# Kernel tuning notes

Measured on AMD Instinct MI355X. Metric: run time of the kernel, lower is better.

Reference implementation:

```python
import jax, jax.numpy as jnp
import numpy as np

N, E = 50000, 800000
NI, NH, NO, NA = 64, 64, 64, 8
C_WEIGHT = 1.0


def psi(p):
    return jnp.sign(p) * jnp.log(jnp.abs(p) + 1.0)


def batchnorm(x, gamma, beta, eps=1e-5):
    # torch BatchNorm1d (training mode): biased variance over the batch dim
    mu = jnp.mean(x, axis=0)
    var = jnp.var(x, axis=0)
    return (x - mu) / jnp.sqrt(var + eps) * gamma + beta


def setup_inputs() -> dict:
    key = jax.random.key(0)
    ks = jax.random.split(key, 16)
    f32 = jnp.float32

    def w(k, shape, s):
        return jax.random.normal(k, shape, dtype=f32) * s

    inp = {}
    inp["h"] = jax.random.normal(ks[0], (N, NI), dtype=f32)
    inp["x"] = jax.random.normal(ks[1], (N, 4), dtype=f32)
    inp["edge_i"] = jax.random.randint(ks[2], (E,), 0, N)
    inp["edge_j"] = jax.random.randint(ks[3], (E,), 0, N)
    inp["node_attr"] = jax.random.normal(ks[4], (N, NA), dtype=f32)
    # phi_e: Linear(2*NI+2 -> NH, no bias), BN, ReLU, Linear(NH -> NH), ReLU
    inp["W_e1"] = w(ks[5], (2 * NI + 2, NH), 0.1)
    inp["g_e"] = jnp.ones((NH,), f32)
    inp["b_e"] = jnp.zeros((NH,), f32)
    inp["W_e2"] = w(ks[6], (NH, NH), 0.1)
    inp["b_e2"] = jnp.zeros((NH,), f32)
    # phi_m: Linear(NH -> 1), Sigmoid
    inp["W_m"] = w(ks[7], (NH, 1), 0.1)
    inp["b_m"] = jnp.zeros((1,), f32)
    # phi_x: Linear(NH -> NH), ReLU, Linear(NH -> 1, no bias, xavier gain=0.001)
    inp["W_x1"] = w(ks[8], (NH, NH), 0.1)
    inp["b_x1"] = jnp.zeros((NH,), f32)
    inp["W_x2"] = w(ks[9], (NH, 1), 0.0003)
    # phi_h: Linear(NH+NI+NA -> NH), BN, ReLU, Linear(NH -> NO)
    inp["W_h1"] = w(ks[10], (NH + NI + NA, NH), 0.1)
    inp["b_h1"] = jnp.zeros((NH,), f32)
    inp["g_h"] = jnp.ones((NH,), f32)
    inp["b_h"] = jnp.zeros((NH,), f32)
    inp["W_h2"] = w(ks[11], (NH, NO), 0.1)
    inp["b_h2"] = jnp.zeros((NO,), f32)
    return inp


def reference(h, x, edge_i, edge_j, node_attr,
              W_e1, g_e, b_e, W_e2, b_e2,
              W_m, b_m, W_x1, b_x1, W_x2,
              W_h1, b_h1, g_h, b_h, W_h2, b_h2):
    n_nodes = h.shape[0]
    xi = x[edge_i]            # [E, 4]
    xj = x[edge_j]            # [E, 4]
    x_diff = xi - xj
    # Minkowski norm / dot: 2*p0*q0 - sum(p*q)
    psq = x_diff * x_diff
    norms = psi(2.0 * psq[:, 0] - psq.sum(axis=-1))[:, None]   # [E,1]
    pq = xi * xj
    dots = psi(2.0 * pq[:, 0] - pq.sum(axis=-1))[:, None]      # [E,1]
    # m_model
    feat = jnp.concatenate([h[edge_i], h[edge_j], norms, dots], axis=1)  # [E, 2*NI+2]
    out = jax.nn.relu(batchnorm(feat @ W_e1, g_e, b_e))
    out = jax.nn.relu(out @ W_e2 + b_e2)
    w_gate = jax.nn.sigmoid(out @ W_m + b_m)
    m = out * w_gate                                            # [E, NH]
    # x_model
    phx = jax.nn.relu(m @ W_x1 + b_x1) @ W_x2                   # [E, 1]
    trans = jnp.clip(x_diff * phx, -100.0, 100.0)
    agg_x = jax.ops.segment_sum(trans, edge_i, num_segments=n_nodes)
    cnt = jax.ops.segment_sum(jnp.ones((trans.shape[0],), trans.dtype),
                              edge_i, num_segments=n_nodes)
    x_new = x + (agg_x / jnp.maximum(cnt, 1.0)[:, None]) * C_WEIGHT
    # h_model
    agg_h = jax.ops.segment_sum(m, edge_i, num_segments=n_nodes)
    hin = jnp.concatenate([h, agg_h, node_attr], axis=1)        # [N, NH+NI+NA]
    hh = jax.nn.relu(batchnorm(hin @ W_h1 + b_h1, g_h, b_h))
    h_new = h + (hh @ W_h2 + b_h2)
    return (h_new, x_new, m)
```

## Files before the change

### kernel.cpp

```cpp
#include <hip/hip_runtime.h>
#include <stdint.h>

typedef __attribute__((ext_vector_type(8))) short bf16x8;
typedef __attribute__((ext_vector_type(4))) float f32x4;

static constexpr int NN = 50000;
static constexpr int NE = 800000;

static constexpr int O_ESUM = 0;
static constexpr int O_ESQ  = 64;
static constexpr int O_HSUM = 128;
static constexpr int O_HSQ  = 192;
static constexpr int O_CNT  = 512;
static constexpr int O_ROW  = O_CNT + 50048;
static constexpr int O_CUR  = O_ROW + 50048;
static constexpr int O_BSUM = O_CUR + 50048;
static constexpr int O_CSR  = O_BSUM + 64;
static constexpr int O_PHX  = O_CSR + NE;
static constexpr int O_AGGH = O_PHX + NE;
static constexpr int O_YH   = O_AGGH + NN*64;
static constexpr int O_PQ   = O_YH + NN*64;
static constexpr int O_YB   = O_PQ + NN*64;
static constexpr int O_ND   = O_YB + NE*32;

static constexpr int OUT_X = NN*64;
static constexpr int OUT_M = NN*64 + NN*4;

__device__ __forceinline__ short f2bf(float f){
  uint32_t u = __builtin_bit_cast(uint32_t, f);
  u = (u + 0x7fffu + ((u >> 16) & 1u)) >> 16;
  return (short)u;
}
__device__ __forceinline__ float bflo(uint32_t w){ return __builtin_bit_cast(float, w << 16); }
__device__ __forceinline__ float bfhi(uint32_t w){ return __builtin_bit_cast(float, w & 0xffff0000u); }
__device__ __forceinline__ float psi_f(float p){
  return copysignf(__logf(fabsf(p) + 1.0f), p);
}
__device__ __forceinline__ bf16x8 ldrow8(const float* p){
  float4 p0 = *(const float4*)p;
  float4 p1 = *(const float4*)(p + 4);
  bf16x8 a;
  a[0]=f2bf(p0.x); a[1]=f2bf(p0.y); a[2]=f2bf(p0.z); a[3]=f2bf(p0.w);
  a[4]=f2bf(p1.x); a[5]=f2bf(p1.y); a[6]=f2bf(p1.z); a[7]=f2bf(p1.w);
  return a;
}

__global__ __launch_bounds__(256) void k_pq(
    const float* __restrict__ h, const float* __restrict__ We1,
    ushort* __restrict__ P, ushort* __restrict__ Q,
    int* __restrict__ cnt, float* __restrict__ wsf)
{
  __shared__ __align__(16) ushort sT[4][1024];
  const int lane = threadIdx.x & 63, wid = threadIdx.x >> 6;
  const int g = lane >> 4, q = lane & 15;
  const int ro = lane >> 2, cb = lane & 3;

  if (blockIdx.x == 0 && threadIdx.x < 256) wsf[threadIdx.x] = 0.f;

  bf16x8 wt[2][4], wm[2][4];
#pragma unroll
  for (int kb=0;kb<2;kb++)
#pragma unroll
    for (int nb=0;nb<4;nb++)
#pragma unroll
      for (int j=0;j<8;j++){
        wt[kb][nb][j] = f2bf(We1[(32*kb + 8*g + j)*64 + 16*nb + q]);
        wm[kb][nb][j] = f2bf(We1[(64 + 32*kb + 8*g + j)*64 + 16*nb + q]);
      }

  ushort* tb = sT[wid];
  const int gw = blockIdx.x*4 + wid, nw = gridDim.x*4;
  for (int t = gw; t < NN/16; t += nw){
    const int rb = t*16;
    if (lane < 16) cnt[rb + lane] = 0;
    const float* hp = h + (size_t)(rb+q)*64;
    bf16x8 a[2];
    a[0] = ldrow8(hp + 8*g); a[1] = ldrow8(hp + 32 + 8*g);

    f32x4 accP[4], accQ[4];
#pragma unroll
    for (int nb=0;nb<4;nb++){ accP[nb] = (f32x4){0.f,0.f,0.f,0.f}; accQ[nb] = (f32x4){0.f,0.f,0.f,0.f}; }
#pragma unroll
    for (int kb=0;kb<2;kb++)
#pragma unroll
      for (int nb=0;nb<4;nb++){
        accP[nb] = __builtin_amdgcn_mfma_f32_16x16x32_bf16(a[kb], wt[kb][nb], accP[nb], 0,0,0);
        accQ[nb] = __builtin_amdgcn_mfma_f32_16x16x32_bf16(a[kb], wm[kb][nb], accQ[nb], 0,0,0);
      }

    asm volatile("s_waitcnt lgkmcnt(0)" ::: "memory");
#pragma unroll
    for (int nb=0;nb<4;nb++)
#pragma unroll
      for (int r=0;r<4;r++){
        const int mr = 4*g + r;
        tb[mr*64 + ((16*nb + q) ^ ((mr&7)<<3))] = (ushort)f2bf(accP[nb][r]);
      }
    asm volatile("s_waitcnt lgkmcnt(0)" ::: "memory");
    {
      const int s = ro & 7;
      uint4 c0 = *(const uint4*)(tb + ro*64 + ((cb*16    ) ^ (s<<3)));
      uint4 c1 = *(const uint4*)(tb + ro*64 + ((cb*16 + 8) ^ (s<<3)));
      *(uint4*)(P + (size_t)(rb+ro)*64 + cb*16    ) = c0;
      *(uint4*)(P + (size_t)(rb+ro)*64 + cb*16 + 8) = c1;
    }
    asm volatile("s_waitcnt lgkmcnt(0)" ::: "memory");
#pragma unroll
    for (int nb=0;nb<4;nb++)
#pragma unroll
      for (int r=0;r<4;r++){
        const int mr = 4*g + r;
        tb[mr*64 + ((16*nb + q) ^ ((mr&7)<<3))] = (ushort)f2bf(accQ[nb][r]);
      }
    asm volatile("s_waitcnt lgkmcnt(0)" ::: "memory");
    {
      const int s = ro & 7;
      uint4 c0 = *(const uint4*)(tb + ro*64 + ((cb*16    ) ^ (s<<3)));
      uint4 c1 = *(const uint4*)(tb + ro*64 + ((cb*16 + 8) ^ (s<<3)));
      *(uint4*)(Q + (size_t)(rb+ro)*64 + cb*16    ) = c0;
      *(uint4*)(Q + (size_t)(rb+ro)*64 + cb*16 + 8) = c1;
    }
  }
}

__global__ __launch_bounds__(256) void k_nd(
    const float* __restrict__ x,
    const int* __restrict__ ei, const int* __restrict__ ej,
    float2* __restrict__ nd, int* __restrict__ cnt)
{
  const int stride = gridDim.x*256;
  for (int e = blockIdx.x*256 + threadIdx.x; e < NE; e += stride){
    const int i = ei[e], j = ej[e];
    const float4 xi = *(const float4*)(x + 4*i);
    const float4 xj = *(const float4*)(x + 4*j);
    const float dx=xi.x-xj.x, dy=xi.y-xj.y, dz=xi.z-xj.z, dw=xi.w-xj.w;
    float2 v;
    v.x = psi_f(dx*dx - dy*dy - dz*dz - dw*dw);
    v.y = psi_f(xi.x*xj.x - xi.y*xj.y - xi.z*xj.z - xi.w*xj.w);
    nd[e] = v;
    atomicAdd(cnt + i, 1);
  }
}

__global__ __launch_bounds__(256) void k_e1(
    const ushort* __restrict__ P, const ushort* __restrict__ Q,
    const int* __restrict__ ei, const int* __restrict__ ej,
    const float2* __restrict__ nd,
    const float* __restrict__ We1,
    ushort* __restrict__ yb, float* __restrict__ wsf)
{
  __shared__ float sred[8][64];
  const int lane = threadIdx.x & 63, wid = threadIdx.x >> 6;
  const float wn = We1[128*64 + lane];
  const float wd = We1[129*64 + lane];
  float ssum = 0.f, ssq = 0.f;

  const int gw = blockIdx.x*4 + wid, nw = gridDim.x*4;
  for (int t = gw; t < NE/8; t += nw){
    const int eb = __builtin_amdgcn_readfirstlane(t*8);
    int iv[8], jv[8];
    float nr[8], dt[8];
#pragma unroll
    for (int k=0;k<8;k++){
      iv[k] = ei[eb+k];
      jv[k] = ej[eb+k];
      const float2 v = nd[eb+k];
      nr[k] = v.x; dt[k] = v.y;
    }
    uint32_t pv[8], qv[8];
#pragma unroll
    for (int k=0;k<8;k++) pv[k] = P[(size_t)iv[k]*64 + lane];
#pragma unroll
    for (int k=0;k<8;k++) qv[k] = Q[(size_t)jv[k]*64 + lane];
#pragma unroll
    for (int k=0;k<8;k++){
      const float y = bflo(pv[k]) + bflo(qv[k]) + nr[k]*wn + dt[k]*wd;
      ssum += y; ssq += y*y;
      yb[(size_t)(eb+k)*64 + lane] = (ushort)f2bf(y);
    }
  }
  sred[wid][lane] = ssum;
  sred[4+wid][lane] = ssq;
  __syncthreads();
  if (wid == 0){
    const float s = sred[0][lane]+sred[1][lane]+sred[2][lane]+sred[3][lane];
    const float z = sred[4][lane]+sred[5][lane]+sred[6][lane]+sred[7][lane];
    atomicAdd(wsf + O_ESUM + lane, s);
    atomicAdd(wsf + O_ESQ  + lane, z);
  }
}

__global__ __launch_bounds__(1024) void k_scan_a(const int* __restrict__ cnt, int* __restrict__ row1,
                                                 int* __restrict__ bsum, int n){
  int v = blockIdx.x*1024 + threadIdx.x;
  int x = (v < n) ? cnt[v] : 0;
  const int lane = threadIdx.x & 63, wid = threadIdx.x >> 6;
#pragma unroll
  for (int d=1; d<64; d<<=1){ int y = __shfl_up(x, d, 64); if (lane >= d) x += y; }
  __shared__ int ws[16];
  if (lane == 63) ws[wid] = x;
  __syncthreads();
  if (wid == 0){
    int s = (lane < 16) ? ws[lane] : 0;
#pragma unroll
    for (int d=1; d<16; d<<=1){ int y = __shfl_up(s, d, 64); if (lane >= d) s += y; }
    if (lane < 16) ws[lane] = s;
  }
  __syncthreads();
  if (wid > 0) x += ws[wid-1];
  if (v < n) row1[v] = x;
  if (threadIdx.x == 1023) bsum[blockIdx.x] = x;
}

__global__ void k_scan_b(int* __restrict__ bsum, int nb){
  int t = threadIdx.x;
  int s = (t < nb) ? bsum[t] : 0;
#pragma unroll
  for (int d=1; d<64; d<<=1){ int y = __shfl_up(s, d, 64); if (t >= d) s += y; }
  if (t < nb) bsum[t] = s;
}

__global__ __launch_bounds__(1024) void k_scan_c(const int* __restrict__ cnt, int* __restrict__ row,
                                                 int* __restrict__ cur, const int* __restrict__ bsum, int n){
  int v = blockIdx.x*1024 + threadIdx.x;
  if (v == 0) row[0] = 0;
  if (v < n){
    int off = (blockIdx.x > 0) ? bsum[blockIdx.x-1] : 0;
    int incl = row[v+1] + off;
    row[v+1] = incl;
    cur[v] = incl - cnt[v];
  }
}

__global__ __launch_bounds__(256) void k_scatter(const int* __restrict__ ei, int* __restrict__ cur,
                                                 int* __restrict__ csr){
  int e = blockIdx.x*256 + threadIdx.x;
  if (e < NE){ int v = ei[e]; int p = atomicAdd(cur + v, 1); csr[p] = e; }
}

__global__ __launch_bounds__(256) void k_e2(
    const ushort* __restrict__ yb,
    const float* __restrict__ ge, const float* __restrict__ be,
    const float* __restrict__ We2, const float* __restrict__ be2,
    const float* __restrict__ Wm, const float* __restrict__ bm,
    const float* __restrict__ Wx1, const float* __restrict__ bx1, const float* __restrict__ Wx2,
    const float* __restrict__ wsf, float* __restrict__ outm, float* __restrict__ phx)
{
  __shared__ uint4 sW[1024];
  __shared__ __align__(16) ushort sT[4][1024];
  __shared__ float sES[64], sEH[64];

  const int tid = threadIdx.x;
  const int lane = tid & 63, wid = tid >> 6;
  const int g = lane >> 4, q = lane & 15;

  if (tid < 64){
    const float mu  = wsf[O_ESUM + tid] * (1.0f/(float)NE);
    const float var = wsf[O_ESQ  + tid] * (1.0f/(float)NE) - mu*mu;
    const float sc  = ge[tid] * rsqrtf(var + 1e-5f);
    sES[tid] = sc;
    sEH[tid] = be[tid] - mu*sc;
  }
  for (int idx = tid; idx < 1024; idx += 256){
    const float* Wsrc = (idx < 512) ? We2 : Wx1;
    const int base = idx & 511;
    const int c = base >> 6, L = base & 63;
    const int kb = c >> 2, nb = c & 3;
    const int Lg = L >> 4, Ln = L & 15;
    uint32_t w[8];
#pragma unroll
    for (int j=0;j<8;j++)
      w[j] = (uint32_t)(uint16_t)f2bf(Wsrc[(32*kb + 8*Lg + j)*64 + 16*nb + Ln]);
    uint4 u;
    u.x = w[0] | (w[1]<<16); u.y = w[2] | (w[3]<<16);
    u.z = w[4] | (w[5]<<16); u.w = w[6] | (w[7]<<16);
    sW[idx] = u;
  }
  __syncthreads();

  float sc2[2][8], sh2[2][8];
#pragma unroll
  for (int kb=0;kb<2;kb++)
#pragma unroll
    for (int j=0;j<8;j++){
      const int ch = 32*kb + 8*g + j;
      sc2[kb][j] = sES[ch];
      sh2[kb][j] = sEH[ch];
    }
  float vbe2[4], vbx1[4], vwm[4], vwx2[4];
#pragma unroll
  for (int nb=0;nb<4;nb++){
    const int c = 16*nb + q;
    vbe2[nb] = be2[c]; vbx1[nb] = bx1[c];
    vwm[nb] = Wm[c];  vwx2[nb] = Wx2[c];
  }
  const float bmv = bm[0];
  ushort* tb = sT[wid];

  const int gw = blockIdx.x*4 + wid, nw = gridDim.x*4;
  for (int t = gw; t < NE/16; t += nw){
    const int eb = t*16;

    bf16x8 a2[2];
#pragma unroll
    for (int kb=0;kb<2;kb++){
      const uint4 raw = *(const uint4*)(yb + (size_t)(eb+q)*64 + 32*kb + 8*g);
      const uint32_t w[4] = {raw.x, raw.y, raw.z, raw.w};
#pragma unroll
      for (int p2=0;p2<4;p2++){
        float v0 = fmaxf(bflo(w[p2])*sc2[kb][2*p2]   + sh2[kb][2*p2],   0.f);
        float v1 = fmaxf(bfhi(w[p2])*sc2[kb][2*p2+1] + sh2[kb][2*p2+1], 0.f);
        a2[kb][2*p2]   = f2bf(v0);
        a2[kb][2*p2+1] = f2bf(v1);
      }
    }

    f32x4 acc2[4];
#pragma unroll
    for (int nb=0;nb<4;nb++){ acc2[nb][0]=vbe2[nb]; acc2[nb][1]=vbe2[nb]; acc2[nb][2]=vbe2[nb]; acc2[nb][3]=vbe2[nb]; }
#pragma unroll
    for (int kb=0;kb<2;kb++)
#pragma unroll
      for (int nb=0;nb<4;nb++)
        acc2[nb] = __builtin_amdgcn_mfma_f32_16x16x32_bf16(
            a2[kb], __builtin_bit_cast(bf16x8, sW[(kb*4+nb)*64 + lane]), acc2[nb], 0,0,0);

    float o2[4][4];
#pragma unroll
    for (int nb=0;nb<4;nb++)
#pragma unroll
      for (int r=0;r<4;r++)
        o2[nb][r] = fmaxf(acc2[nb][r], 0.f);

    float gate[4];
#pragma unroll
    for (int r=0;r<4;r++){
      float s = o2[0][r]*vwm[0] + o2[1][r]*vwm[1] + o2[2][r]*vwm[2] + o2[3][r]*vwm[3];
      s += __shfl_xor(s,1,64); s += __shfl_xor(s,2,64);
      s += __shfl_xor(s,4,64); s += __shfl_xor(s,8,64);
      gate[r] = 1.f/(1.f + __expf(-(s + bmv)));
    }

    float mv[4][4];
#pragma unroll
    for (int nb=0;nb<4;nb++)
#pragma unroll
      for (int r=0;r<4;r++){
        mv[nb][r] = o2[nb][r]*gate[r];
        outm[(size_t)(eb + 4*g + r)*64 + 16*nb + q] = mv[nb][r];
      }

    asm volatile("s_waitcnt lgkmcnt(0)" ::: "memory");
#pragma unroll
    for (int nb=0;nb<4;nb++)
#pragma unroll
      for (int r=0;r<4;r++){
        const int mr = 4*g + r;
        tb[mr*64 + ((16*nb + q) ^ ((mr&7)<<3))] = (ushort)f2bf(mv[nb][r]);
      }
    asm volatile("s_waitcnt lgkmcnt(0)" ::: "memory");
    bf16x8 a3[2];
#pragma unroll
    for (int kb=0;kb<2;kb++){
      const int k0 = 32*kb + 8*g;
      uint4 uv = *(const uint4*)(tb + q*64 + (k0 ^ ((q&7)<<3)));
      a3[kb] = __builtin_bit_cast(bf16x8, uv);
    }

    f32x4 acc3[4];
#pragma unroll
    for (int nb=0;nb<4;nb++){ acc3[nb][0]=vbx1[nb]; acc3[nb][1]=vbx1[nb]; acc3[nb][2]=vbx1[nb]; acc3[nb][3]=vbx1[nb]; }
#pragma unroll
    for (int kb=0;kb<2;kb++)
#pragma unroll
      for (int nb=0;nb<4;nb++)
        acc3[nb] = __builtin_amdgcn_mfma_f32_16x16x32_bf16(
            a3[kb], __builtin_bit_cast(bf16x8, sW[512 + (kb*4+nb)*64 + lane]), acc3[nb], 0,0,0);

    float pd[4];
#pragma unroll
    for (int r=0;r<4;r++){
      float s = fmaxf(acc3[0][r],0.f)*vwx2[0] + fmaxf(acc3[1][r],0.f)*vwx2[1]
              + fmaxf(acc3[2][r],0.f)*vwx2[2] + fmaxf(acc3[3][r],0.f)*vwx2[3];
      s += __shfl_xor(s,1,64); s += __shfl_xor(s,2,64);
      s += __shfl_xor(s,4,64); s += __shfl_xor(s,8,64);
      pd[r] = s;
    }
    if (q == 0){
#pragma unroll
      for (int r=0;r<4;r++) phx[eb + 4*g + r] = pd[r];
    }
  }
}

__global__ __launch_bounds__(256) void k_agg(
    const float* __restrict__ x, const int* __restrict__ ej,
    const int* __restrict__ row, const int* __restrict__ csr,
    const float* __restrict__ m, const float* __restrict__ phx,
    float* __restrict__ aggh, float* __restrict__ out)
{
  const int lane = threadIdx.x & 63, wid = threadIdx.x >> 6;
  const int comp = lane & 3, eoff = lane >> 2;
  const int gw = blockIdx.x*4 + wid, nw = gridDim.x*4;
  for (int v = gw; v < NN; v += nw){
    const int s  = __builtin_amdgcn_readfirstlane(row[v]);
    const int e1 = __builtin_amdgcn_readfirstlane(row[v+1]);

    float ah = 0.f;
    int p = s;
    for (; p + 8 <= e1; p += 8){
      const int c0=csr[p+0], c1=csr[p+1], c2=csr[p+2], c3=csr[p+3];
      const int c4=csr[p+4], c5=csr[p+5], c6=csr[p+6], c7=csr[p+7];
      const float v0 = m[(size_t)c0*64 + lane];
      const float v1 = m[(size_t)c1*64 + lane];
      const float v2 = m[(size_t)c2*64 + lane];
      const float v3 = m[(size_t)c3*64 + lane];
      const float v4 = m[(size_t)c4*64 + lane];
      const float v5 = m[(size_t)c5*64 + lane];
      const float v6 = m[(size_t)c6*64 + lane];
      const float v7 = m[(size_t)c7*64 + lane];
      ah += ((v0+v1)+(v2+v3)) + ((v4+v5)+(v6+v7));
    }
    for (; p < e1; ++p) ah += m[(size_t)csr[p]*64 + lane];
    aggh[(size_t)v*64 + lane] = ah;

    const float xv = x[4*v + comp];
    float ax = 0.f;
    for (int p2 = s; p2 < e1; p2 += 16){
      const int idx = p2 + eoff;
      if (idx < e1){
        const int e = csr[idx];
        const int j = ej[e];
        float tr = (xv - x[4*j + comp]) * phx[e];
        ax += fminf(fmaxf(tr, -100.f), 100.f);
      }
    }
    ax += __shfl_xor(ax, 4, 64);
    ax += __shfl_xor(ax, 8, 64);
    ax += __shfl_xor(ax,16, 64);
    ax += __shfl_xor(ax,32, 64);
    if (lane < 4){
      const float deg = (float)(e1 - s);
      out[OUT_X + 4*v + lane] = xv + ax / fmaxf(deg, 1.f);
    }
  }
}

__global__ __launch_bounds__(256) void k_h1(
    const float* __restrict__ h, const float* __restrict__ aggh, const float* __restrict__ attr,
    const float* __restrict__ Wh1, float* __restrict__ yh, float* __restrict__ wsf)
{
  const int lane = threadIdx.x & 63, wid = threadIdx.x >> 6;
  const int g = lane >> 4, q = lane & 15;

  bf16x8 wf[4][4];
#pragma unroll
  for (int kb=0;kb<4;kb++)
#pragma unroll
    for (int nb=0;nb<4;nb++)
#pragma unroll
      for (int j=0;j<8;j++)
        wf[kb][nb][j] = f2bf(Wh1[(32*kb + 8*g + j)*64 + 16*nb + q]);
  float wa[8][4];
#pragma unroll
  for (int a8=0;a8<8;a8++)
#pragma unroll
    for (int nb=0;nb<4;nb++)
      wa[a8][nb] = Wh1[(128+a8)*64 + 16*nb + q];

  float ssum[4]={0.f,0.f,0.f,0.f}, ssq[4]={0.f,0.f,0.f,0.f};
  const int gw = blockIdx.x*4 + wid, nw = gridDim.x*4;
  for (int t = gw; t < NN/16; t += nw){
    const int rb = t*16;
    bf16x8 a[4];
    const float* hp = h    + (size_t)(rb+q)*64;
    const float* ap = aggh + (size_t)(rb+q)*64;
    a[0]=ldrow8(hp + 8*g); a[1]=ldrow8(hp + 32 + 8*g);
    a[2]=ldrow8(ap + 8*g); a[3]=ldrow8(ap + 32 + 8*g);

    float at[4][8];
#pragma unroll
    for (int r=0;r<4;r++){
      const float* pp = attr + (size_t)(rb + 4*g + r)*8;
      float4 p0 = *(const float4*)pp; float4 p1 = *(const float4*)(pp + 4);
      at[r][0]=p0.x; at[r][1]=p0.y; at[r][2]=p0.z; at[r][3]=p0.w;
      at[r][4]=p1.x; at[r][5]=p1.y; at[r][6]=p1.z; at[r][7]=p1.w;
    }
    f32x4 acc[4];
#pragma unroll
    for (int nb=0;nb<4;nb++)
#pragma unroll
      for (int r=0;r<4;r++){
        float ci = 0.f;
#pragma unroll
        for (int a8=0;a8<8;a8++) ci += at[r][a8]*wa[a8][nb];
        acc[nb][r] = ci;
      }
#pragma unroll
    for (int kb=0;kb<4;kb++)
#pragma unroll
      for (int nb=0;nb<4;nb++)
        acc[nb] = __builtin_amdgcn_mfma_f32_16x16x32_bf16(a[kb], wf[kb][nb], acc[nb], 0,0,0);

#pragma unroll
    for (int nb=0;nb<4;nb++)
#pragma unroll
      for (int r=0;r<4;r++){
        float v = acc[nb][r];
        yh[(size_t)(rb + 4*g + r)*64 + 16*nb + q] = v;
        ssum[nb] += v; ssq[nb] += v*v;
      }
  }
#pragma unroll
  for (int nb=0;nb<4;nb++){
    float s = ssum[nb], z = ssq[nb];
    s += __shfl_xor(s,16,64); s += __shfl_xor(s,32,64);
    z += __shfl_xor(z,16,64); z += __shfl_xor(z,32,64);
    if (lane < 16){
      atomicAdd(wsf + O_HSUM + 16*nb + lane, s);
      atomicAdd(wsf + O_HSQ  + 16*nb + lane, z);
    }
  }
}

__global__ __launch_bounds__(256) void k_h2(
    const float* __restrict__ h, const float* __restrict__ yh,
    const float* __restrict__ gh, const float* __restrict__ bh,
    const float* __restrict__ Wh2, const float* __restrict__ bh2,
    const float* __restrict__ wsf, float* __restrict__ out)
{
  __shared__ float sHS[64], sHH[64];
  const int tid = threadIdx.x;
  const int lane = tid & 63, wid = tid >> 6;
  const int g = lane >> 4, q = lane & 15;

  if (tid < 64){
    const float mu  = wsf[O_HSUM + tid] * (1.0f/(float)NN);
    const float var = wsf[O_HSQ  + tid] * (1.0f/(float)NN) - mu*mu;
    const float sc  = gh[tid] * rsqrtf(var + 1e-5f);
    sHS[tid] = sc;
    sHH[tid] = bh[tid] - mu*sc;
  }
  __syncthreads();

  bf16x8 wf[2][4];
#pragma unroll
  for (int kb=0;kb<2;kb++)
#pragma unroll
    for (int nb=0;nb<4;nb++)
#pragma unroll
      for (int j=0;j<8;j++)
        wf[kb][nb][j] = f2bf(Wh2[(32*kb + 8*g + j)*64 + 16*nb + q]);

  float sc[2][8], sh[2][8];
#pragma unroll
  for (int kb=0;kb<2;kb++)
#pragma unroll
    for (int j=0;j<8;j++){
      const int k = 32*kb + 8*g + j;
      sc[kb][j] = sHS[k]; sh[kb][j] = sHH[k];
    }
  float vb[4];
#pragma unroll
  for (int nb=0;nb<4;nb++) vb[nb] = bh2[16*nb + q];

  const int gw = blockIdx.x*4 + wid, nw = gridDim.x*4;
  for (int t = gw; t < NN/16; t += nw){
    const int rb = t*16;
    const float* yp = yh + (size_t)(rb+q)*64;
    bf16x8 a[2];
#pragma unroll
    for (int kb=0;kb<2;kb++){
      float4 p0 = *(const float4*)(yp + 32*kb + 8*g);
      float4 p1 = *(const float4*)(yp + 32*kb + 8*g + 4);
      float v[8] = {p0.x,p0.y,p0.z,p0.w,p1.x,p1.y,p1.z,p1.w};
#pragma unroll
      for (int j=0;j<8;j++)
        a[kb][j] = f2bf(fmaxf(v[j]*sc[kb][j] + sh[kb][j], 0.f));
    }
    f32x4 acc[4];
#pragma unroll
    for (int nb=0;nb<4;nb++){ acc[nb][0]=vb[nb]; acc[nb][1]=vb[nb]; acc[nb][2]=vb[nb]; acc[nb][3]=vb[nb]; }
#pragma unroll
    for (int kb=0;kb<2;kb++)
#pragma unroll
      for (int nb=0;nb<4;nb++)
        acc[nb] = __builtin_amdgcn_mfma_f32_16x16x32_bf16(a[kb], wf[kb][nb], acc[nb], 0,0,0);

#pragma unroll
    for (int nb=0;nb<4;nb++)
#pragma unroll
      for (int r=0;r<4;r++){
        const size_t idx = (size_t)(rb + 4*g + r)*64 + 16*nb + q;
        out[idx] = h[idx] + acc[nb][r];
      }
  }
}

extern "C" void kernel_launch(void* const* d_in, const int* in_sizes, int n_in,
                              void* d_out, int out_size, void* d_ws, size_t ws_size,
                              hipStream_t stream){
  const float* h    = (const float*)d_in[0];
  const float* x    = (const float*)d_in[1];
  const int*   ei   = (const int*)d_in[2];
  const int*   ej   = (const int*)d_in[3];
  const float* attr = (const float*)d_in[4];
  const float* We1  = (const float*)d_in[5];
  const float* ge   = (const float*)d_in[6];
  const float* be   = (const float*)d_in[7];
  const float* We2  = (const float*)d_in[8];
  const float* be2  = (const float*)d_in[9];
  const float* Wm   = (const float*)d_in[10];
  const float* bm   = (const float*)d_in[11];
  const float* Wx1  = (const float*)d_in[12];
  const float* bx1  = (const float*)d_in[13];
  const float* Wx2  = (const float*)d_in[14];
  const float* Wh1  = (const float*)d_in[15];
  const float* gh   = (const float*)d_in[17];
  const float* bh   = (const float*)d_in[18];
  const float* Wh2  = (const float*)d_in[19];
  const float* bh2  = (const float*)d_in[20];

  float* out = (float*)d_out;
  float* wsf = (float*)d_ws;
  int*   wsi = (int*)d_ws;
  ushort* P  = (ushort*)(wsf + O_PQ);
  ushort* Q  = P + (size_t)NN*64;
  ushort* yb = (ushort*)(wsf + O_YB);
  float2* nd = (float2*)(wsf + O_ND);

  k_pq<<<256,256,0,stream>>>(h, We1, P, Q, wsi+O_CNT, wsf);
  k_nd<<<2048,256,0,stream>>>(x, ei, ej, nd, wsi+O_CNT);
  k_e1<<<2048,256,0,stream>>>(P, Q, ei, ej, nd, We1, yb, wsf);
  k_scan_a<<<49,1024,0,stream>>>(wsi+O_CNT, wsi+O_ROW+1, wsi+O_BSUM, NN);
  k_scan_b<<<1,64,0,stream>>>(wsi+O_BSUM, 49);
  k_scan_c<<<49,1024,0,stream>>>(wsi+O_CNT, wsi+O_ROW, wsi+O_CUR, wsi+O_BSUM, NN);
  k_scatter<<<(NE+255)/256,256,0,stream>>>(ei, wsi+O_CUR, wsi+O_CSR);
  k_e2<<<1024,256,0,stream>>>(yb, ge, be, We2, be2, Wm, bm, Wx1, bx1, Wx2,
                              wsf, out + OUT_M, wsf + O_PHX);
  k_agg<<<2048,256,0,stream>>>(x, ej, wsi+O_ROW, wsi+O_CSR, out + OUT_M, wsf + O_PHX,
                               wsf + O_AGGH, out);
  k_h1<<<256,256,0,stream>>>(h, wsf + O_AGGH, attr, Wh1, wsf + O_YH, wsf);
  k_h2<<<256,256,0,stream>>>(h, wsf + O_YH, gh, bh, Wh2, bh2, wsf, out);
}
```

Before: 395.0 us.

## Process edges in CSR order and fuse segment aggregation into edge MLP kernel

Edges are now processed in destination-sorted (CSR) order in k_e1/k_e2, so consecutive rows usually share a destination node. The per-node aggregation of m and the x-translation is folded into k_e2 through wave-level pre-reduction and atomic adds, and the separate k_agg gather kernel is removed. A small k_xf kernel does the final x division. This removes the gather-reread of m and phx, at the cost of indirect edge-index loads, scattered m stores, float atomics and an extra xd buffer written in k_nd.

```diff
diff --git a/kernel.cpp b/kernel.cpp
--- a/kernel.cpp
+++ b/kernel.cpp
@@ -16,12 +16,13 @@
 static constexpr int O_CUR  = O_ROW + 50048;
 static constexpr int O_BSUM = O_CUR + 50048;
 static constexpr int O_CSR  = O_BSUM + 64;
-static constexpr int O_PHX  = O_CSR + NE;
-static constexpr int O_AGGH = O_PHX + NE;
+static constexpr int O_AX   = O_CSR + NE;
+static constexpr int O_XD   = O_AX + 200192;
+static constexpr int O_ND   = O_XD + NE*4;
+static constexpr int O_AGGH = O_ND + NE*2;
 static constexpr int O_YH   = O_AGGH + NN*64;
 static constexpr int O_PQ   = O_YH + NN*64;
 static constexpr int O_YB   = O_PQ + NN*64;
-static constexpr int O_ND   = O_YB + NE*32;
 
 static constexpr int OUT_X = NN*64;
 static constexpr int OUT_M = NN*64 + NN*4;
@@ -57,6 +58,9 @@
 
   if (blockIdx.x == 0 && threadIdx.x < 256) wsf[threadIdx.x] = 0.f;
 
+  float* aggh = wsf + O_AGGH;
+  float* axb  = wsf + O_AX;
+
   bf16x8 wt[2][4], wm[2][4];
 #pragma unroll
   for (int kb=0;kb<2;kb++)
@@ -73,6 +77,10 @@
   for (int t = gw; t < NN/16; t += nw){
     const int rb = t*16;
     if (lane < 16) cnt[rb + lane] = 0;
+    axb[rb*4 + lane] = 0.f;
+#pragma unroll
+    for (int k=0;k<16;k++) aggh[(size_t)(rb+k)*64 + lane] = 0.f;
+
     const float* hp = h + (size_t)(rb+q)*64;
     bf16x8 a[2];
     a[0] = ldrow8(hp + 8*g); a[1] = ldrow8(hp + 32 + 8*g);
@@ -126,7 +134,7 @@
 __global__ __launch_bounds__(256) void k_nd(
     const float* __restrict__ x,
     const int* __restrict__ ei, const int* __restrict__ ej,
-    float2* __restrict__ nd, int* __restrict__ cnt)
+    float2* __restrict__ nd, float4* __restrict__ xd, int* __restrict__ cnt)
 {
   const int stride = gridDim.x*256;
   for (int e = blockIdx.x*256 + threadIdx.x; e < NE; e += stride){
@@ -138,12 +146,63 @@
     v.x = psi_f(dx*dx - dy*dy - dz*dz - dw*dw);
     v.y = psi_f(xi.x*xj.x - xi.y*xj.y - xi.z*xj.z - xi.w*xj.w);
     nd[e] = v;
+    float4 d; d.x=dx; d.y=dy; d.z=dz; d.w=dw;
+    xd[e] = d;
     atomicAdd(cnt + i, 1);
   }
+}
+
+__global__ __launch_bounds__(1024) void k_scan_a(const int* __restrict__ cnt, int* __restrict__ row1,
+                                                 int* __restrict__ bsum, int n){
+  int v = blockIdx.x*1024 + threadIdx.x;
+  int x = (v < n) ? cnt[v] : 0;
+  const int lane = threadIdx.x & 63, wid = threadIdx.x >> 6;
+#pragma unroll
+  for (int d=1; d<64; d<<=1){ int y = __shfl_up(x, d, 64); if (lane >= d) x += y; }
+  __shared__ int ws[16];
+  if (lane == 63) ws[wid] = x;
+  __syncthreads();
+  if (wid == 0){
+    int s = (lane < 16) ? ws[lane] : 0;
+#pragma unroll
+    for (int d=1; d<16; d<<=1){ int y = __shfl_up(s, d, 64); if (lane >= d) s += y; }
+    if (lane < 16) ws[lane] = s;
+  }
+  __syncthreads();
+  if (wid > 0) x += ws[wid-1];
+  if (v < n) row1[v] = x;
+  if (threadIdx.x == 1023) bsum[blockIdx.x] = x;
+}
+
+__global__ void k_scan_b(int* __restrict__ bsum, int nb){
+  int t = threadIdx.x;
+  int s = (t < nb) ? bsum[t] : 0;
+#pragma unroll
+  for (int d=1; d<64; d<<=1){ int y = __shfl_up(s, d, 64); if (t >= d) s += y; }
+  if (t < nb) bsum[t] = s;
+}
+
+__global__ __launch_bounds__(1024) void k_scan_c(const int* __restrict__ cnt, int* __restrict__ row,
+                                                 int* __restrict__ cur, const int* __restrict__ bsum, int n){
+  int v = blockIdx.x*1024 + threadIdx.x;
+  if (v == 0) row[0] = 0;
+  if (v < n){
+    int off = (blockIdx.x > 0) ? bsum[blockIdx.x-1] : 0;
+    int incl = row[v+1] + off;
+    row[v+1] = incl;
+    cur[v] = incl - cnt[v];
+  }
+}
+
+__global__ __launch_bounds__(256) void k_scatter(const int* __restrict__ ei, int* __restrict__ cur,
+                                                 int* __restrict__ csr){
+  int e = blockIdx.x*256 + threadIdx.x;
+  if (e < NE){ int v = ei[e]; int p = atomicAdd(cur + v, 1); csr[p] = e; }
 }
 
 __global__ __launch_bounds__(256) void k_e1(
     const ushort* __restrict__ P, const ushort* __restrict__ Q,
+    const int* __restrict__ csr,
     const int* __restrict__ ei, const int* __restrict__ ej,
     const float2* __restrict__ nd,
     const float* __restrict__ We1,
@@ -157,14 +216,17 @@
 
   const int gw = blockIdx.x*4 + wid, nw = gridDim.x*4;
   for (int t = gw; t < NE/8; t += nw){
-    const int eb = __builtin_amdgcn_readfirstlane(t*8);
-    int iv[8], jv[8];
+    const int pb = __builtin_amdgcn_readfirstlane(t*8);
+    int ev[8], iv[8], jv[8];
     float nr[8], dt[8];
 #pragma unroll
+    for (int k=0;k<8;k++)
+      ev[k] = __builtin_amdgcn_readfirstlane(csr[pb+k]);
+#pragma unroll
     for (int k=0;k<8;k++){
-      iv[k] = ei[eb+k];
-      jv[k] = ej[eb+k];
-      const float2 v = nd[eb+k];
+      iv[k] = ei[ev[k]];
+      jv[k] = ej[ev[k]];
+      const float2 v = nd[ev[k]];
       nr[k] = v.x; dt[k] = v.y;
     }
     uint32_t pv[8], qv[8];
@@ -176,7 +238,7 @@
     for (int k=0;k<8;k++){
       const float y = bflo(pv[k]) + bflo(qv[k]) + nr[k]*wn + dt[k]*wd;
       ssum += y; ssq += y*y;
-      yb[(size_t)(eb+k)*64 + lane] = (ushort)f2bf(y);
+      yb[(size_t)(pb+k)*64 + lane] = (ushort)f2bf(y);
     }
   }
   sred[wid][lane] = ssum;
@@ -190,65 +252,23 @@
   }
 }
 
-__global__ __launch_bounds__(1024) void k_scan_a(const int* __restrict__ cnt, int* __restrict__ row1,
-                                                 int* __restrict__ bsum, int n){
-  int v = blockIdx.x*1024 + threadIdx.x;
-  int x = (v < n) ? cnt[v] : 0;
-  const int lane = threadIdx.x & 63, wid = threadIdx.x >> 6;
-#pragma unroll
-  for (int d=1; d<64; d<<=1){ int y = __shfl_up(x, d, 64); if (lane >= d) x += y; }
-  __shared__ int ws[16];
-  if (lane == 63) ws[wid] = x;
-  __syncthreads();
-  if (wid == 0){
-    int s = (lane < 16) ? ws[lane] : 0;
-#pragma unroll
-    for (int d=1; d<16; d<<=1){ int y = __shfl_up(s, d, 64); if (lane >= d) s += y; }
-    if (lane < 16) ws[lane] = s;
-  }
-  __syncthreads();
-  if (wid > 0) x += ws[wid-1];
-  if (v < n) row1[v] = x;
-  if (threadIdx.x == 1023) bsum[blockIdx.x] = x;
-}
-
-__global__ void k_scan_b(int* __restrict__ bsum, int nb){
-  int t = threadIdx.x;
-  int s = (t < nb) ? bsum[t] : 0;
-#pragma unroll
-  for (int d=1; d<64; d<<=1){ int y = __shfl_up(s, d, 64); if (t >= d) s += y; }
-  if (t < nb) bsum[t] = s;
-}
-
-__global__ __launch_bounds__(1024) void k_scan_c(const int* __restrict__ cnt, int* __restrict__ row,
-                                                 int* __restrict__ cur, const int* __restrict__ bsum, int n){
-  int v = blockIdx.x*1024 + threadIdx.x;
-  if (v == 0) row[0] = 0;
-  if (v < n){
-    int off = (blockIdx.x > 0) ? bsum[blockIdx.x-1] : 0;
-    int incl = row[v+1] + off;
-    row[v+1] = incl;
-    cur[v] = incl - cnt[v];
-  }
-}
-
-__global__ __launch_bounds__(256) void k_scatter(const int* __restrict__ ei, int* __restrict__ cur,
-                                                 int* __restrict__ csr){
-  int e = blockIdx.x*256 + threadIdx.x;
-  if (e < NE){ int v = ei[e]; int p = atomicAdd(cur + v, 1); csr[p] = e; }
-}
-
 __global__ __launch_bounds__(256) void k_e2(
-    const ushort* __restrict__ yb,
+    const ushort* __restrict__ yb, const int* __restrict__ csr, const int* __restrict__ ei,
+    const float* __restrict__ xd,
     const float* __restrict__ ge, const float* __restrict__ be,
     const float* __restrict__ We2, const float* __restrict__ be2,
     const float* __restrict__ Wm, const float* __restrict__ bm,
     const float* __restrict__ Wx1, const float* __restrict__ bx1, const float* __restrict__ Wx2,
-    const float* __restrict__ wsf, float* __restrict__ outm, float* __restrict__ phx)
+    const float* __restrict__ wsf, float* __restrict__ outm,
+    float* __restrict__ aggh, float* __restrict__ axb)
 {
   __shared__ uint4 sW[1024];
   __shared__ __align__(16) ushort sT[4][1024];
   __shared__ float sES[64], sEH[64];
+  __shared__ int   sEID[4][16];
+  __shared__ int   sNID[4][16];
+  __shared__ float sPD[4][16];
+  __shared__ float sXD[4][64];
 
   const int tid = threadIdx.x;
   const int lane = tid & 63, wid = tid >> 6;
@@ -301,6 +321,12 @@
   for (int t = gw; t < NE/16; t += nw){
     const int eb = t*16;
 
+    if (lane < 16){
+      const int e = csr[eb + lane];
+      sEID[wid][lane] = e;
+      sNID[wid][lane] = ei[e];
+    }
+
     bf16x8 a2[2];
 #pragma unroll
     for (int kb=0;kb<2;kb++){
@@ -341,13 +367,20 @@
       gate[r] = 1.f/(1.f + __expf(-(s + bmv)));
     }
 
+    int e_row[4], n_row[4];
+#pragma unroll
+    for (int r=0;r<4;r++){
+      e_row[r] = sEID[wid][4*g + r];
+      n_row[r] = sNID[wid][4*g + r];
+    }
+
     float mv[4][4];
 #pragma unroll
     for (int nb=0;nb<4;nb++)
 #pragma unroll
       for (int r=0;r<4;r++){
         mv[nb][r] = o2[nb][r]*gate[r];
-        outm[(size_t)(eb + 4*g + r)*64 + 16*nb + q] = mv[nb][r];
+        outm[(size_t)e_row[r]*64 + 16*nb + q] = mv[nb][r];
       }
 
     asm volatile("s_waitcnt lgkmcnt(0)" ::: "memory");
@@ -388,61 +421,62 @@
     }
     if (q == 0){
 #pragma unroll
-      for (int r=0;r<4;r++) phx[eb + 4*g + r] = pd[r];
-    }
-  }
-}
-
-__global__ __launch_bounds__(256) void k_agg(
-    const float* __restrict__ x, const int* __restrict__ ej,
-    const int* __restrict__ row, const int* __restrict__ csr,
-    const float* __restrict__ m, const float* __restrict__ phx,
-    float* __restrict__ aggh, float* __restrict__ out)
+      for (int r=0;r<4;r++) sPD[wid][4*g + r] = pd[r];
+    }
+    {
+      const int rr = lane >> 2;
+      sXD[wid][lane] = xd[(size_t)sEID[wid][rr]*4 + (lane & 3)];
+    }
+
+#pragma unroll 1
+    for (int k=0;k<16;k++){
+      const int nk = __builtin_amdgcn_readfirstlane(sNID[wid][k]);
+      if (k > 0 && nk == __builtin_amdgcn_readfirstlane(sNID[wid][k-1])) continue;
+      float tot[4] = {0.f,0.f,0.f,0.f};
+#pragma unroll
+      for (int r=0;r<4;r++){
+        if (n_row[r] == nk){
+#pragma unroll
+          for (int nb=0;nb<4;nb++) tot[nb] += mv[nb][r];
+        }
+      }
+#pragma unroll
+      for (int nb=0;nb<4;nb++){
+        tot[nb] += __shfl_xor(tot[nb],16,64);
+        tot[nb] += __shfl_xor(tot[nb],32,64);
+      }
+      if (lane < 16){
+#pragma unroll
+        for (int nb=0;nb<4;nb++)
+          atomicAdd(aggh + (size_t)nk*64 + 16*nb + q, tot[nb]);
+      }
+      float axs = 0.f;
+      if (q < 4){
+#pragma unroll
+        for (int r=0;r<4;r++){
+          if (n_row[r] == nk){
+            const int rr = 4*g + r;
+            float tr = sXD[wid][rr*4 + q] * sPD[wid][rr];
+            axs += fminf(fmaxf(tr, -100.f), 100.f);
+          }
+        }
+      }
+      axs += __shfl_xor(axs,16,64);
+      axs += __shfl_xor(axs,32,64);
+      if (lane < 4) atomicAdd(axb + (size_t)nk*4 + lane, axs);
+    }
+  }
+}
+
+__global__ __launch_bounds__(256) void k_xf(
+    const float* __restrict__ x, const int* __restrict__ row,
+    const float* __restrict__ axb, float* __restrict__ out)
 {
-  const int lane = threadIdx.x & 63, wid = threadIdx.x >> 6;
-  const int comp = lane & 3, eoff = lane >> 2;
-  const int gw = blockIdx.x*4 + wid, nw = gridDim.x*4;
-  for (int v = gw; v < NN; v += nw){
-    const int s  = __builtin_amdgcn_readfirstlane(row[v]);
-    const int e1 = __builtin_amdgcn_readfirstlane(row[v+1]);
-
-    float ah = 0.f;
-    int p = s;
-    for (; p + 8 <= e1; p += 8){
-      const int c0=csr[p+0], c1=csr[p+1], c2=csr[p+2], c3=csr[p+3];
-      const int c4=csr[p+4], c5=csr[p+5], c6=csr[p+6], c7=csr[p+7];
-      const float v0 = m[(size_t)c0*64 + lane];
-      const float v1 = m[(size_t)c1*64 + lane];
-      const float v2 = m[(size_t)c2*64 + lane];
-      const float v3 = m[(size_t)c3*64 + lane];
-      const float v4 = m[(size_t)c4*64 + lane];
-      const float v5 = m[(size_t)c5*64 + lane];
-      const float v6 = m[(size_t)c6*64 + lane];
-      const float v7 = m[(size_t)c7*64 + lane];
-      ah += ((v0+v1)+(v2+v3)) + ((v4+v5)+(v6+v7));
-    }
-    for (; p < e1; ++p) ah += m[(size_t)csr[p]*64 + lane];
-    aggh[(size_t)v*64 + lane] = ah;
-
-    const float xv = x[4*v + comp];
-    float ax = 0.f;
-    for (int p2 = s; p2 < e1; p2 += 16){
-      const int idx = p2 + eoff;
-      if (idx < e1){
-        const int e = csr[idx];
-        const int j = ej[e];
-        float tr = (xv - x[4*j + comp]) * phx[e];
-        ax += fminf(fmaxf(tr, -100.f), 100.f);
-      }
-    }
-    ax += __shfl_xor(ax, 4, 64);
-    ax += __shfl_xor(ax, 8, 64);
-    ax += __shfl_xor(ax,16, 64);
-    ax += __shfl_xor(ax,32, 64);
-    if (lane < 4){
-      const float deg = (float)(e1 - s);
-      out[OUT_X + 4*v + lane] = xv + ax / fmaxf(deg, 1.f);
-    }
+  int t = blockIdx.x*256 + threadIdx.x;
+  if (t < NN*4){
+    const int v = t >> 2;
+    const float deg = (float)(row[v+1] - row[v]);
+    out[OUT_X + t] = x[t] + axb[t] / fmaxf(deg, 1.f);
   }
 }
 
@@ -628,18 +662,19 @@
   ushort* Q  = P + (size_t)NN*64;
   ushort* yb = (ushort*)(wsf + O_YB);
   float2* nd = (float2*)(wsf + O_ND);
+  float4* xd = (float4*)(wsf + O_XD);
 
   k_pq<<<256,256,0,stream>>>(h, We1, P, Q, wsi+O_CNT, wsf);
-  k_nd<<<2048,256,0,stream>>>(x, ei, ej, nd, wsi+O_CNT);
-  k_e1<<<2048,256,0,stream>>>(P, Q, ei, ej, nd, We1, yb, wsf);
+  k_nd<<<2048,256,0,stream>>>(x, ei, ej, nd, xd, wsi+O_CNT);
   k_scan_a<<<49,1024,0,stream>>>(wsi+O_CNT, wsi+O_ROW+1, wsi+O_BSUM, NN);
   k_scan_b<<<1,64,0,stream>>>(wsi+O_BSUM, 49);
   k_scan_c<<<49,1024,0,stream>>>(wsi+O_CNT, wsi+O_ROW, wsi+O_CUR, wsi+O_BSUM, NN);
   k_scatter<<<(NE+255)/256,256,0,stream>>>(ei, wsi+O_CUR, wsi+O_CSR);
-  k_e2<<<1024,256,0,stream>>>(yb, ge, be, We2, be2, Wm, bm, Wx1, bx1, Wx2,
-                              wsf, out + OUT_M, wsf + O_PHX);
-  k_agg<<<2048,256,0,stream>>>(x, ej, wsi+O_ROW, wsi+O_CSR, out + OUT_M, wsf + O_PHX,
-                               wsf + O_AGGH, out);
+  k_e1<<<2048,256,0,stream>>>(P, Q, wsi+O_CSR, ei, ej, nd, We1, yb, wsf);
+  k_e2<<<1024,256,0,stream>>>(yb, wsi+O_CSR, ei, (const float*)(wsf+O_XD),
+                              ge, be, We2, be2, Wm, bm, Wx1, bx1, Wx2,
+                              wsf, out + OUT_M, wsf + O_AGGH, wsf + O_AX);
+  k_xf<<<(NN*4+255)/256,256,0,stream>>>(x, wsi+O_ROW, wsf+O_AX, out);
   k_h1<<<256,256,0,stream>>>(h, wsf + O_AGGH, attr, Wh1, wsf + O_YH, wsf);
   k_h2<<<256,256,0,stream>>>(h, wsf + O_YH, gh, bh, Wh2, bh2, wsf, out);
 }
```

After: 499.0 us. +26.4%, slower.
